# Performance work log

Hardware: AMD Instinct MI355X
Metric: run time of the kernel (lower is better)

The kernel has to match this reference:

```python
import jax, jax.numpy as jnp
import numpy as np
from jax import lax


def setup_inputs() -> dict:
    key = jax.random.key(0)
    ks = jax.random.split(key, 11)
    B, S, V, E, H = 32, 256, 32000, 128, 128
    return {
        "sequence": jax.random.randint(ks[0], (B, S), 0, V),
        "encoder_output": jax.random.normal(ks[1], (B, S, H), jnp.float32),
        "encoder_output_hidden": jax.random.normal(ks[2], (1, B, H), jnp.float32),
        "encoder_output_cell": jax.random.normal(ks[3], (1, B, H), jnp.float32),
        "emb": jax.random.normal(ks[4], (V, E), jnp.float32) * 0.02,
        "W_ih": jax.random.normal(ks[5], (4 * H, E + H), jnp.float32) * 0.05,
        "b_ih": jax.random.normal(ks[6], (4 * H,), jnp.float32) * 0.05,
        "W_hh": jax.random.normal(ks[7], (4 * H, H), jnp.float32) * 0.05,
        "b_hh": jax.random.normal(ks[8], (4 * H,), jnp.float32) * 0.05,
        "W_pred": jax.random.normal(ks[9], (V, H), jnp.float32) * 0.05,
        "b_pred": jax.random.normal(ks[10], (V,), jnp.float32) * 0.05,
    }


def reference(sequence, encoder_output, encoder_output_hidden, encoder_output_cell,
              emb, W_ih, b_ih, W_hh, b_hh, W_pred, b_pred):
    B, S = sequence.shape
    H = W_hh.shape[1]
    x = emb[sequence]                      # [B, S, E]
    h0 = encoder_output_hidden[0]          # [B, H] fixed state fed every step
    c0 = encoder_output_cell[0]            # [B, H]
    # gate contribution from the fixed hidden state is constant over time
    hh = h0 @ W_hh.T + b_hh                # [B, 4H]

    def step(h_prev, x_t):
        inp = jnp.concatenate([x_t, h_prev], axis=1)   # [B, E+H]
        gates = inp @ W_ih.T + b_ih + hh               # [B, 4H]
        i, f, g, o = jnp.split(gates, 4, axis=1)       # torch LSTMCell order
        c = jax.nn.sigmoid(f) * c0 + jax.nn.sigmoid(i) * jnp.tanh(g)
        h = jax.nn.sigmoid(o) * jnp.tanh(c)
        return h, h

    h_init = jnp.zeros((B, H), x.dtype)
    _, hs = lax.scan(step, h_init, jnp.swapaxes(x, 0, 1))  # hs: [S, B, H]
    hs = jnp.swapaxes(hs, 0, 1)                            # [B, S, H]
    logits = hs @ W_pred.T + b_pred                        # [B, S, V]
    return jax.nn.log_softmax(logits, axis=-1)
```

## Files before the change

### kernel.cpp

```cpp
#include <hip/hip_runtime.h>

typedef short bf16x8 __attribute__((ext_vector_type(8)));
typedef float f32x4  __attribute__((ext_vector_type(4)));
typedef unsigned short u16;
typedef unsigned short u16x8 __attribute__((ext_vector_type(8)));

#define NB   32
#define NS   256
#define NV   32000
#define NE   128
#define NH   128
#define NR   8192
#define NG   512
#define NCHUNK 500

__device__ __forceinline__ float sigm(float x){
    return __builtin_amdgcn_rcpf(1.0f + __expf(-x));
}
__device__ __forceinline__ float tanh_fast(float x){
    return 1.0f - 2.0f*__builtin_amdgcn_rcpf(1.0f + __expf(2.0f*x));
}

__device__ __forceinline__ u16 f2bf(float x){
    unsigned u = __float_as_uint(x);
    unsigned r = (u + 0x7FFFu + ((u >> 16) & 1u)) >> 16;
    return (u16)r;
}

__device__ __forceinline__ void lds_barrier(){
    asm volatile("s_waitcnt lgkmcnt(0)" ::: "memory");
    __builtin_amdgcn_s_barrier();
    __builtin_amdgcn_sched_barrier(0);
}

__global__ __launch_bounds__(256) void khh(const float* __restrict__ h0,
                                           const float* __restrict__ W_hh,
                                           const float* __restrict__ b_ih,
                                           const float* __restrict__ b_hh,
                                           float* __restrict__ hh){
    int idx = blockIdx.x*256 + threadIdx.x;
    int b = idx >> 9, j = idx & 511;
    const float4* h4 = (const float4*)(h0 + b*NH);
    const float4* w4 = (const float4*)(W_hh + j*NH);
    float acc = b_ih[j] + b_hh[j];
    #pragma unroll
    for (int k = 0; k < 32; ++k){
        float4 a = h4[k], w = w4[k];
        acc += a.x*w.x + a.y*w.y + a.z*w.z + a.w*w.w;
    }
    hh[idx] = acc;
}

__global__ __launch_bounds__(256) void kwb(const float* __restrict__ src, u16* __restrict__ dst){
    int i = (blockIdx.x*256 + threadIdx.x)*8;
    float4 a = *(const float4*)(src + i);
    float4 b = *(const float4*)(src + i + 4);
    u16x8 o;
    o[0]=f2bf(a.x); o[1]=f2bf(a.y); o[2]=f2bf(a.z); o[3]=f2bf(a.w);
    o[4]=f2bf(b.x); o[5]=f2bf(b.y); o[6]=f2bf(b.z); o[7]=f2bf(b.w);
    *(u16x8*)(dst + i) = o;
}

__global__ __launch_bounds__(256) void kxg(const int* __restrict__ seq,
                                           const float* __restrict__ emb,
                                           const float* __restrict__ W_ih,
                                           float* __restrict__ xg){
    __shared__ float4 xs[16][32];
    int m0 = blockIdx.x * 16;
    int t = threadIdx.x;
    int r = t >> 4, k4 = t & 15;
    int tok = seq[m0 + r];
    xs[r][k4]      = *(const float4*)(emb + (size_t)tok*NE + k4*4);
    xs[r][k4 + 16] = *(const float4*)(emb + (size_t)tok*NE + (k4+16)*4);
    __syncthreads();
    int j0 = t, j1 = t + 256;
    const float4* w0 = (const float4*)(W_ih + (size_t)j0*256);
    const float4* w1 = (const float4*)(W_ih + (size_t)j1*256);
    float acc0[16], acc1[16];
    #pragma unroll
    for (int r2 = 0; r2 < 16; ++r2){ acc0[r2]=0.f; acc1[r2]=0.f; }
    #pragma unroll
    for (int k = 0; k < 32; ++k){
        float4 wa = w0[k], wb = w1[k];
        #pragma unroll
        for (int r2 = 0; r2 < 16; ++r2){
            float4 xv = xs[r2][k];
            acc0[r2] += xv.x*wa.x + xv.y*wa.y + xv.z*wa.z + xv.w*wa.w;
            acc1[r2] += xv.x*wb.x + xv.y*wb.y + xv.z*wb.z + xv.w*wb.w;
        }
    }
    #pragma unroll
    for (int r2 = 0; r2 < 16; ++r2){
        xg[(size_t)(m0+r2)*NG + j0] = acc0[r2];
        xg[(size_t)(m0+r2)*NG + j1] = acc1[r2];
    }
}

__global__ __launch_bounds__(256, 1) void klstm(const float* __restrict__ xg,
                                                const float* __restrict__ hh,
                                                const float* __restrict__ W_ih,
                                                const float* __restrict__ c0,
                                                u16* __restrict__ hs){
    __shared__ __align__(16) unsigned hsh2[2][64];
    int b = blockIdx.x, t = threadIdx.x;
    int r = t >> 1, odd = t & 1;
    int gA = r + (odd ? 128 : 0);
    int gB = gA + 256;
    unsigned w2a[64], w2b[64];
    const float2* wra = (const float2*)(W_ih + (size_t)gA*256 + 128);
    const float2* wrb = (const float2*)(W_ih + (size_t)gB*256 + 128);
    #pragma unroll
    for (int k = 0; k < 64; ++k){
        float2 va = wra[k], vb = wrb[k];
        w2a[k] = ((unsigned)f2bf(va.y) << 16) | (unsigned)f2bf(va.x);
        w2b[k] = ((unsigned)f2bf(vb.y) << 16) | (unsigned)f2bf(vb.x);
    }
    float hba = hh[b*NG + gA];
    float hbb = hh[b*NG + gB];
    float c0r = c0[b*NH + r];
    if (t < 64){ hsh2[0][t] = 0u; }
    __syncthreads();
    const float* xrow = xg + (size_t)b*NS*NG;
    u16* hrow = hs + (size_t)b*NS*NH;
    float xva = xrow[gA], xvb = xrow[gB];
    for (int s = 0; s < NS; ++s){
        float xna = 0.f, xnb = 0.f;
        if (s+1 < NS){ xna = xrow[(size_t)(s+1)*NG + gA]; xnb = xrow[(size_t)(s+1)*NG + gB]; }
        float a0=0.f,a1=0.f,a2=0.f,a3=0.f,b0=0.f,b1=0.f,b2=0.f,b3=0.f;
        const uint4* h4 = (const uint4*)&hsh2[s & 1][0];
        #pragma unroll
        for (int k = 0; k < 16; ++k){
            uint4 hv = h4[k];
            asm("v_dot2_f32_bf16 %0, %1, %2, %0" : "+v"(a0) : "v"(hv.x), "v"(w2a[4*k+0]));
            asm("v_dot2_f32_bf16 %0, %1, %2, %0" : "+v"(a1) : "v"(hv.y), "v"(w2a[4*k+1]));
            asm("v_dot2_f32_bf16 %0, %1, %2, %0" : "+v"(a2) : "v"(hv.z), "v"(w2a[4*k+2]));
            asm("v_dot2_f32_bf16 %0, %1, %2, %0" : "+v"(a3) : "v"(hv.w), "v"(w2a[4*k+3]));
            asm("v_dot2_f32_bf16 %0, %1, %2, %0" : "+v"(b0) : "v"(hv.x), "v"(w2b[4*k+0]));
            asm("v_dot2_f32_bf16 %0, %1, %2, %0" : "+v"(b1) : "v"(hv.y), "v"(w2b[4*k+1]));
            asm("v_dot2_f32_bf16 %0, %1, %2, %0" : "+v"(b2) : "v"(hv.z), "v"(w2b[4*k+2]));
            asm("v_dot2_f32_bf16 %0, %1, %2, %0" : "+v"(b3) : "v"(hv.w), "v"(w2b[4*k+3]));
        }
        float gateA = hba + xva + ((a0+a1)+(a2+a3));
        float gateB = hbb + xvb + ((b0+b1)+(b2+b3));
        float fg = __shfl_xor(gateA, 1);
        float og = __shfl_xor(gateB, 1);
        float cc = sigm(fg)*c0r + sigm(gateA)*tanh_fast(gateB);
        float h  = sigm(og)*tanh_fast(cc);
        u16 hb16 = f2bf(h);
        if (!odd) hrow[s*NH + r] = hb16;
        unsigned hpart = __shfl_xor((unsigned)hb16, 2);
        if ((t & 3) == 0) hsh2[(s & 1) ^ 1][r >> 1] = (hpart << 16) | (unsigned)hb16;
        lds_barrier();
        xva = xna; xvb = xnb;
    }
}

template<int PASS>
__global__ __launch_bounds__(256, 2) void kgemm(const u16* __restrict__ hsb,
                                                const u16* __restrict__ wb,
                                                const float* __restrict__ bpred,
                                                const float* __restrict__ lse,
                                                float* __restrict__ psum,
                                                float* __restrict__ out){
    extern __shared__ char smem[];
    u16* Al = (u16*)smem;
    u16* Bl = Al + 128*136;
    int tid = threadIdx.x;
    int bid = blockIdx.x;
    int c    = bid >> 1;
    int half = bid & 1;
    int n0 = c * 128;
    int mbase = half * 4096;

    uint4 breg[8];
    #pragma unroll
    for (int i = 0; i < 8; ++i){
        int flat = tid + 256*i; int row = flat >> 4, ch = flat & 15;
        breg[i] = *(const uint4*)&wb[(size_t)(n0+row)*NH + ch*8];
    }
    uint4 areg[8];
    #pragma unroll
    for (int i = 0; i < 8; ++i){
        int flat = tid + 256*i; int row = flat >> 4, ch = flat & 15;
        areg[i] = *(const uint4*)&hsb[(size_t)(mbase + row)*NH + ch*8];
    }
    #pragma unroll
    for (int i = 0; i < 8; ++i){
        int flat = tid + 256*i; int row = flat >> 4, ch = flat & 15;
        *(uint4*)&Bl[row*136 + ch*8] = breg[i];
    }
    #pragma unroll
    for (int i = 0; i < 8; ++i){
        int flat = tid + 256*i; int row = flat >> 4, ch = flat & 15;
        *(uint4*)&Al[row*136 + ch*8] = areg[i];
    }
    __syncthreads();

    int wid = tid >> 6, lane = tid & 63;
    int wr = wid >> 1, wc = wid & 1;
    int l15 = lane & 15, l4 = lane >> 4;
    const float L2E = 1.44269504f;
    float4 bp4[4], bpl4[4];
    #pragma unroll
    for (int f = 0; f < 4; ++f){
        bp4[f] = *(const float4*)&bpred[n0 + wc*64 + f*16 + l4*4];
        bpl4[f].x = bp4[f].x * L2E; bpl4[f].y = bp4[f].y * L2E;
        bpl4[f].z = bp4[f].z * L2E; bpl4[f].w = bp4[f].w * L2E;
    }

    for (int r = 0; r < 32; ++r){
        if (r + 1 < 32){
            #pragma unroll
            for (int i = 0; i < 8; ++i){
                int flat = tid + 256*i; int row = flat >> 4, ch = flat & 15;
                areg[i] = *(const uint4*)&hsb[(size_t)(mbase + (r+1)*128 + row)*NH + ch*8];
            }
        }
        bf16x8 af[4][4];
        #pragma unroll
        for (int q = 0; q < 4; ++q)
            #pragma unroll
            for (int kk = 0; kk < 4; ++kk)
                af[q][kk] = *(const bf16x8*)&Al[(wr*64 + q*16 + l15)*136 + kk*32 + l4*8];
        f32x4 acc[4][4];
        #pragma unroll
        for (int q = 0; q < 4; ++q)
            #pragma unroll
            for (int f = 0; f < 4; ++f)
                acc[q][f] = (f32x4){0.f,0.f,0.f,0.f};
        #pragma unroll
        for (int f = 0; f < 4; ++f){
            bf16x8 bfr[4];
            #pragma unroll
            for (int kk = 0; kk < 4; ++kk)
                bfr[kk] = *(const bf16x8*)&Bl[(wc*64 + f*16 + l15)*136 + kk*32 + l4*8];
            #pragma unroll
            for (int q = 0; q < 4; ++q)
                #pragma unroll
                for (int kk = 0; kk < 4; ++kk)
                    acc[q][f] = __builtin_amdgcn_mfma_f32_16x16x32_bf16(bfr[kk], af[q][kk], acc[q][f], 0, 0, 0);
        }

        lds_barrier();
        if (r + 1 < 32){
            #pragma unroll
            for (int i = 0; i < 8; ++i){
                int flat = tid + 256*i; int row = flat >> 4, ch = flat & 15;
                *(uint4*)&Al[row*136 + ch*8] = areg[i];
            }
        }

        if (PASS == 0){
            float lsum[4];
            #pragma unroll
            for (int q = 0; q < 4; ++q){
                float s = 0.f;
                #pragma unroll
                for (int f = 0; f < 4; ++f)
                    #pragma unroll
                    for (int rr = 0; rr < 4; ++rr){
                        float tt = fmaf(acc[q][f][rr], L2E, bpl4[f][rr]);
                        float e; asm("v_exp_f32 %0, %1" : "=v"(e) : "v"(tt));
                        s += e;
                    }
                s += __shfl_xor(s, 16);
                s += __shfl_xor(s, 32);
                lsum[q] = s;
            }
            float sv = (l4 == 0) ? lsum[0] : (l4 == 1) ? lsum[1]
                     : (l4 == 2) ? lsum[2] : lsum[3];
            psum[(size_t)(c*2 + wc)*NR + mbase + r*128 + wr*64 + lane] = sv;
        } else {
            #pragma unroll
            for (int q = 0; q < 4; ++q){
                int grow = mbase + r*128 + wr*64 + q*16 + l15;
                float lw = lse[grow];
                float* orow = out + (size_t)grow*NV + n0 + wc*64 + l4*4;
                #pragma unroll
                for (int f = 0; f < 4; ++f){
                    f32x4 v;
                    v[0] = acc[q][f][0] + bp4[f].x - lw;
                    v[1] = acc[q][f][1] + bp4[f].y - lw;
                    v[2] = acc[q][f][2] + bp4[f].z - lw;
                    v[3] = acc[q][f][3] + bp4[f].w - lw;
                    *(f32x4*)&orow[f*16] = v;
                }
            }
        }
        lds_barrier();
    }
}

__global__ __launch_bounds__(256) void klse(const float* __restrict__ psum,
                                            float* __restrict__ lse){
    int row = blockIdx.x*256 + threadIdx.x;
    float S = 0.f;
    for (int cc = 0; cc < NCHUNK; ++cc) S += psum[(size_t)cc*NR + row];
    lse[row] = __logf(S);
}

extern "C" void kernel_launch(void* const* d_in, const int* in_sizes, int n_in,
                              void* d_out, int out_size, void* d_ws, size_t ws_size,
                              hipStream_t stream){
    (void)in_sizes; (void)n_in; (void)out_size; (void)ws_size;
    const int*   seq    = (const int*)d_in[0];
    const float* h0     = (const float*)d_in[2];
    const float* c0     = (const float*)d_in[3];
    const float* emb    = (const float*)d_in[4];
    const float* W_ih   = (const float*)d_in[5];
    const float* b_ih   = (const float*)d_in[6];
    const float* W_hh   = (const float*)d_in[7];
    const float* b_hh   = (const float*)d_in[8];
    const float* W_pred = (const float*)d_in[9];
    const float* b_pred = (const float*)d_in[10];
    float* out = (float*)d_out;

    char* ws = (char*)d_ws;
    float* xg   = (float*)(ws);
    float* psum = (float*)(ws);
    float* hh   = (float*)(ws + 16777216);
    u16*   hsb  = (u16*)  (ws + 16842752);
    u16*   wbb  = (u16*)  (ws + 18939904);
    float* lse  = (float*)(ws + 27131904);

    khh<<<64, 256, 0, stream>>>(h0, W_hh, b_ih, b_hh, hh);
    kwb<<<2000, 256, 0, stream>>>(W_pred, wbb);
    kxg<<<512, 256, 0, stream>>>(seq, emb, W_ih, xg);
    klstm<<<32, 256, 0, stream>>>(xg, hh, W_ih, c0, hsb);
    kgemm<0><<<500, 256, 69632, stream>>>(hsb, wbb, b_pred, nullptr, psum, out);
    klse<<<32, 256, 0, stream>>>(psum, lse);
    kgemm<1><<<500, 256, 69632, stream>>>(hsb, wbb, b_pred, lse, psum, out);
}
```

Baseline: 685.7 us.

## Load GEMM fragments directly from global into registers, drop LDS staging

```diff
diff --git a/kernel.cpp b/kernel.cpp
--- a/kernel.cpp
+++ b/kernel.cpp
@@ -155,6 +155,71 @@
     }
 }
 
+
+#define LOAD_A(DST, R)                                                          \
+    _Pragma("unroll")                                                           \
+    for (int q = 0; q < 4; ++q){                                                \
+        _Pragma("unroll")                                                       \
+        for (int kk = 0; kk < 4; ++kk)                                          \
+            DST[q][kk] = *(const bf16x8*)&hsb[(size_t)(mbase + (R)*128 + wr*64  \
+                         + q*16 + l15)*NH + kk*32 + l4*8];                      \
+    }
+
+#define DO_TILE(AF, R)                                                          \
+    {                                                                           \
+        f32x4 acc[4][4];                                                        \
+        _Pragma("unroll")                                                       \
+        for (int q = 0; q < 4; ++q)                                             \
+            _Pragma("unroll")                                                   \
+            for (int f = 0; f < 4; ++f)                                         \
+                acc[q][f] = (f32x4){0.f,0.f,0.f,0.f};                           \
+        _Pragma("unroll")                                                       \
+        for (int f = 0; f < 4; ++f)                                             \
+            _Pragma("unroll")                                                   \
+            for (int q = 0; q < 4; ++q)                                         \
+                _Pragma("unroll")                                               \
+                for (int kk = 0; kk < 4; ++kk)                                  \
+                    acc[q][f] = __builtin_amdgcn_mfma_f32_16x16x32_bf16(        \
+                        bfr[f][kk], AF[q][kk], acc[q][f], 0, 0, 0);             \
+        if (PASS == 0){                                                         \
+            float lsum[4];                                                      \
+            _Pragma("unroll")                                                   \
+            for (int q = 0; q < 4; ++q){                                        \
+                float s = 0.f;                                                  \
+                _Pragma("unroll")                                               \
+                for (int f = 0; f < 4; ++f)                                     \
+                    _Pragma("unroll")                                           \
+                    for (int rr = 0; rr < 4; ++rr){                             \
+                        float tt = fmaf(acc[q][f][rr], L2E, bpl4[f][rr]);       \
+                        float e; asm("v_exp_f32 %0, %1" : "=v"(e) : "v"(tt));   \
+                        s += e;                                                 \
+                    }                                                           \
+                s += __shfl_xor(s, 16);                                         \
+                s += __shfl_xor(s, 32);                                         \
+                lsum[q] = s;                                                    \
+            }                                                                   \
+            float sv = (l4 == 0) ? lsum[0] : (l4 == 1) ? lsum[1]                \
+                     : (l4 == 2) ? lsum[2] : lsum[3];                           \
+            psum[(size_t)(c*2 + wc)*NR + mbase + (R)*128 + wr*64 + lane] = sv;  \
+        } else {                                                                \
+            _Pragma("unroll")                                                   \
+            for (int q = 0; q < 4; ++q){                                        \
+                int grow = mbase + (R)*128 + wr*64 + q*16 + l15;                \
+                float lw = lse[grow];                                           \
+                float* orow = out + (size_t)grow*NV + n0 + wc*64 + l4*4;        \
+                _Pragma("unroll")                                               \
+                for (int f = 0; f < 4; ++f){                                    \
+                    f32x4 v;                                                    \
+                    v[0] = acc[q][f][0] + bp4[f].x - lw;                        \
+                    v[1] = acc[q][f][1] + bp4[f].y - lw;                        \
+                    v[2] = acc[q][f][2] + bp4[f].z - lw;                        \
+                    v[3] = acc[q][f][3] + bp4[f].w - lw;                        \
+                    *(f32x4*)&orow[f*16] = v;                                   \
+                }                                                               \
+            }                                                                   \
+        }                                                                       \
+    }
+
 template<int PASS>
 __global__ __launch_bounds__(256, 2) void kgemm(const u16* __restrict__ hsb,
                                                 const u16* __restrict__ wb,
@@ -162,9 +227,6 @@
                                                 const float* __restrict__ lse,
                                                 float* __restrict__ psum,
                                                 float* __restrict__ out){
-    extern __shared__ char smem[];
-    u16* Al = (u16*)smem;
-    u16* Bl = Al + 128*136;
     int tid = threadIdx.x;
     int bid = blockIdx.x;
     int c    = bid >> 1;
@@ -172,30 +234,6 @@
     int n0 = c * 128;
     int mbase = half * 4096;
 
-    uint4 breg[8];
-    #pragma unroll
-    for (int i = 0; i < 8; ++i){
-        int flat = tid + 256*i; int row = flat >> 4, ch = flat & 15;
-        breg[i] = *(const uint4*)&wb[(size_t)(n0+row)*NH + ch*8];
-    }
-    uint4 areg[8];
-    #pragma unroll
-    for (int i = 0; i < 8; ++i){
-        int flat = tid + 256*i; int row = flat >> 4, ch = flat & 15;
-        areg[i] = *(const uint4*)&hsb[(size_t)(mbase + row)*NH + ch*8];
-    }
-    #pragma unroll
-    for (int i = 0; i < 8; ++i){
-        int flat = tid + 256*i; int row = flat >> 4, ch = flat & 15;
-        *(uint4*)&Bl[row*136 + ch*8] = breg[i];
-    }
-    #pragma unroll
-    for (int i = 0; i < 8; ++i){
-        int flat = tid + 256*i; int row = flat >> 4, ch = flat & 15;
-        *(uint4*)&Al[row*136 + ch*8] = areg[i];
-    }
-    __syncthreads();
-
     int wid = tid >> 6, lane = tid & 63;
     int wr = wid >> 1, wc = wid & 1;
     int l15 = lane & 15, l4 = lane >> 4;
@@ -208,86 +246,20 @@
         bpl4[f].z = bp4[f].z * L2E; bpl4[f].w = bp4[f].w * L2E;
     }
 
-    for (int r = 0; r < 32; ++r){
-        if (r + 1 < 32){
-            #pragma unroll
-            for (int i = 0; i < 8; ++i){
-                int flat = tid + 256*i; int row = flat >> 4, ch = flat & 15;
-                areg[i] = *(const uint4*)&hsb[(size_t)(mbase + (r+1)*128 + row)*NH + ch*8];
-            }
-        }
-        bf16x8 af[4][4];
+    bf16x8 bfr[4][4];
+    #pragma unroll
+    for (int f = 0; f < 4; ++f)
         #pragma unroll
-        for (int q = 0; q < 4; ++q)
-            #pragma unroll
-            for (int kk = 0; kk < 4; ++kk)
-                af[q][kk] = *(const bf16x8*)&Al[(wr*64 + q*16 + l15)*136 + kk*32 + l4*8];
-        f32x4 acc[4][4];
-        #pragma unroll
-        for (int q = 0; q < 4; ++q)
-            #pragma unroll
-            for (int f = 0; f < 4; ++f)
-                acc[q][f] = (f32x4){0.f,0.f,0.f,0.f};
-        #pragma unroll
-        for (int f = 0; f < 4; ++f){
-            bf16x8 bfr[4];
-            #pragma unroll
-            for (int kk = 0; kk < 4; ++kk)
-                bfr[kk] = *(const bf16x8*)&Bl[(wc*64 + f*16 + l15)*136 + kk*32 + l4*8];
-            #pragma unroll
-            for (int q = 0; q < 4; ++q)
-                #pragma unroll
-                for (int kk = 0; kk < 4; ++kk)
-                    acc[q][f] = __builtin_amdgcn_mfma_f32_16x16x32_bf16(bfr[kk], af[q][kk], acc[q][f], 0, 0, 0);
-        }
-
-        lds_barrier();
-        if (r + 1 < 32){
-            #pragma unroll
-            for (int i = 0; i < 8; ++i){
-                int flat = tid + 256*i; int row = flat >> 4, ch = flat & 15;
-                *(uint4*)&Al[row*136 + ch*8] = areg[i];
-            }
-        }
-
-        if (PASS == 0){
-            float lsum[4];
-            #pragma unroll
-            for (int q = 0; q < 4; ++q){
-                float s = 0.f;
-                #pragma unroll
-                for (int f = 0; f < 4; ++f)
-                    #pragma unroll
-                    for (int rr = 0; rr < 4; ++rr){
-                        float tt = fmaf(acc[q][f][rr], L2E, bpl4[f][rr]);
-                        float e; asm("v_exp_f32 %0, %1" : "=v"(e) : "v"(tt));
-                        s += e;
-                    }
-                s += __shfl_xor(s, 16);
-                s += __shfl_xor(s, 32);
-                lsum[q] = s;
-            }
-            float sv = (l4 == 0) ? lsum[0] : (l4 == 1) ? lsum[1]
-                     : (l4 == 2) ? lsum[2] : lsum[3];
-            psum[(size_t)(c*2 + wc)*NR + mbase + r*128 + wr*64 + lane] = sv;
-        } else {
-            #pragma unroll
-            for (int q = 0; q < 4; ++q){
-                int grow = mbase + r*128 + wr*64 + q*16 + l15;
-                float lw = lse[grow];
-                float* orow = out + (size_t)grow*NV + n0 + wc*64 + l4*4;
-                #pragma unroll
-                for (int f = 0; f < 4; ++f){
-                    f32x4 v;
-                    v[0] = acc[q][f][0] + bp4[f].x - lw;
-                    v[1] = acc[q][f][1] + bp4[f].y - lw;
-                    v[2] = acc[q][f][2] + bp4[f].z - lw;
-                    v[3] = acc[q][f][3] + bp4[f].w - lw;
-                    *(f32x4*)&orow[f*16] = v;
-                }
-            }
-        }
-        lds_barrier();
+        for (int kk = 0; kk < 4; ++kk)
+            bfr[f][kk] = *(const bf16x8*)&wb[(size_t)(n0 + wc*64 + f*16 + l15)*NH + kk*32 + l4*8];
+
+    bf16x8 afA[4][4], afB[4][4];
+    LOAD_A(afA, 0);
+    for (int r = 0; r < 32; r += 2){
+        LOAD_A(afB, r+1);
+        DO_TILE(afA, r);
+        if (r + 2 < 32) LOAD_A(afA, r+2);
+        DO_TILE(afB, r+1);
     }
 }
 
@@ -327,7 +299,7 @@
     kwb<<<2000, 256, 0, stream>>>(W_pred, wbb);
     kxg<<<512, 256, 0, stream>>>(seq, emb, W_ih, xg);
     klstm<<<32, 256, 0, stream>>>(xg, hh, W_ih, c0, hsb);
-    kgemm<0><<<500, 256, 69632, stream>>>(hsb, wbb, b_pred, nullptr, psum, out);
+    kgemm<0><<<500, 256, 0, stream>>>(hsb, wbb, b_pred, nullptr, psum, out);
     klse<<<32, 256, 0, stream>>>(psum, lse);
-    kgemm<1><<<500, 256, 69632, stream>>>(hsb, wbb, b_pred, lse, psum, out);
-}
+    kgemm<1><<<500, 256, 0, stream>>>(hsb, wbb, b_pred, lse, psum, out);
+}
```

Result: slower. 715.4 us (+4.3%).
